# Optimization experiments

Hardware: AMD Instinct MI355X
Metric: run time of the kernel (lower is better)

Reference implementation:

```python
import jax, jax.numpy as jnp
import numpy as np

N_NODES = 65536
N_EDGES = 524288
N_GRAPHS = 512
G_NODES = 10000
NUM_DISEASES = 2000
IN_DIM = 128
HID = 256  # 2 * IN_DIM (z_emb concat feat)
D_FEAT = 512
C_FEAT = 512
MAX_Z = 4000


def setup_inputs() -> dict:
    key = jax.random.key(0)
    ks = jax.random.split(key, 20)
    rn = lambda k, shape: jax.random.normal(k, shape, dtype=jnp.float32) * 0.05
    return {
        "z": jax.random.randint(ks[0], (N_NODES,), 0, MAX_Z),
        "node_id": jnp.sort(jax.random.randint(ks[1], (N_NODES,), 0, G_NODES)),
        "src": jax.random.randint(ks[2], (N_EDGES,), 0, N_NODES),
        "dst": jax.random.randint(ks[3], (N_EDGES,), 0, N_NODES),
        "graph_ids": jnp.sort(jax.random.randint(ks[4], (N_NODES,), 0, N_GRAPHS)),
        "z_table": rn(ks[5], (MAX_Z, IN_DIM)),
        "d_feat_tab": rn(ks[6], (G_NODES, D_FEAT)),
        "c_feat_tab": rn(ks[7], (G_NODES, C_FEAT)),
        "Wd": rn(ks[8], (D_FEAT, IN_DIM)),
        "Wc": rn(ks[9], (C_FEAT, IN_DIM)),
        "gin_W1": rn(ks[10], (HID, HID)), "gin_b1": jnp.zeros((HID,), jnp.float32),
        "gin_W2": rn(ks[11], (HID, HID)), "gin_b2": jnp.zeros((HID,), jnp.float32),
        "sage_Wself": rn(ks[12], (HID, HID)),
        "sage_Wneigh": rn(ks[13], (HID, HID)),
        "sage_b": jnp.zeros((HID,), jnp.float32),
        "lin1_W": rn(ks[14], (HID, HID)), "lin1_b": jnp.zeros((HID,), jnp.float32),
        "lin2_W": rn(ks[15], (HID, 1)), "lin2_b": jnp.zeros((1,), jnp.float32),
    }


def reference(z, node_id, src, dst, graph_ids, z_table, d_feat_tab, c_feat_tab,
              Wd, Wc, gin_W1, gin_b1, gin_W2, gin_b2,
              sage_Wself, sage_Wneigh, sage_b, lin1_W, lin1_b, lin2_W, lin2_b):
    # --- input feature construction (Model.forward) ---
    z_emb = z_table[z]                               # [N, IN_DIM]
    d_proj = d_feat_tab[node_id] @ Wd                # d_fc (bias=False)
    c_proj = c_feat_tab[node_id] @ Wc                # c_fc (bias=False)
    disease = (node_id <= NUM_DISEASES)[:, None]
    # node_id is sorted -> masked concat order == node order
    feat = jnp.where(disease, d_proj, c_proj)        # [N, IN_DIM]
    x = jnp.concatenate([z_emb, feat], axis=1)       # [N, HID]
    # --- GINConv: sum aggregation, eps=0, mlp = Lin->ReLU->Lin ---
    agg = jax.ops.segment_sum(x[src], dst, num_segments=N_NODES)
    h = x + agg
    h = jax.nn.relu(h @ gin_W1 + gin_b1) @ gin_W2 + gin_b2
    # --- SAGEConv('mean'): fc_self(h) + fc_neigh(mean_neighbors) + bias ---
    deg = jax.ops.segment_sum(jnp.ones((N_EDGES,), h.dtype), dst, num_segments=N_NODES)
    mean_n = jax.ops.segment_sum(h[src], dst, num_segments=N_NODES) / jnp.maximum(deg, 1.0)[:, None]
    h = h @ sage_Wself + mean_n @ sage_Wneigh + sage_b
    # --- per-graph max pooling readout ---
    g = jax.ops.segment_max(h, graph_ids, num_segments=N_GRAPHS, indices_are_sorted=True)
    g = jnp.where(jnp.isfinite(g), g, 0.0)           # guard empty graphs
    # --- head: Linear -> ReLU -> (dropout p=0, eval) -> Linear ---
    h = jax.nn.relu(g @ lin1_W + lin1_b)
    return h @ lin2_W + lin2_b                       # [N_GRAPHS, 1]
```

## Files before the change

### kernel.cpp

```cpp
#include <hip/hip_runtime.h>
#include <hip/hip_bf16.h>

#define N_NODES     65536
#define N_EDGES     524288
#define N_GRAPHS    512
#define G_NODES_N   10000
#define NUM_DIS     2000
#define IN_DIM      128
#define HID         256
#define D_FEAT      512

typedef _Float16 half8 __attribute__((ext_vector_type(8)));
typedef _Float16 half4v __attribute__((ext_vector_type(4)));
typedef float    f32x4 __attribute__((ext_vector_type(4)));

__global__ __launch_bounds__(256) void wcvt_all_kernel(
    const float* __restrict__ W1, const float* __restrict__ W2,
    const float* __restrict__ Ws, const float* __restrict__ Wn,
    const float* __restrict__ Wd, const float* __restrict__ Wc,
    _Float16* __restrict__ W1T, _Float16* __restrict__ W2T,
    _Float16* __restrict__ WsT, _Float16* __restrict__ WnT,
    _Float16* __restrict__ WdT, _Float16* __restrict__ WcT)
{
    int b = blockIdx.x;
    const float* W; _Float16* T; int N, K, n;
    if (b < 1024) {
        const int m = b >> 8; n = b & 255; N = HID; K = HID;
        W = (m == 0) ? W1 : (m == 1) ? W2 : (m == 2) ? Ws : Wn;
        T = (m == 0) ? W1T : (m == 1) ? W2T : (m == 2) ? WsT : WnT;
    } else {
        b -= 1024; const int m = b >> 7; n = b & 127; N = IN_DIM; K = D_FEAT;
        W = (m == 0) ? Wd : Wc;
        T = (m == 0) ? WdT : WcT;
    }
    for (int k = threadIdx.x; k < K; k += 256)
        T[(size_t)n * K + k] = (_Float16)W[(size_t)k * N + n];
}

__global__ __launch_bounds__(256) void proj_mfma_kernel(
    const float* __restrict__ dtab, const float* __restrict__ ctab,
    const _Float16* __restrict__ WdT, const _Float16* __restrict__ WcT,
    _Float16* __restrict__ proj)
{
    __shared__ _Float16 Alds[128 * 40];
    __shared__ _Float16 Blds[128 * 40];
    const int blk = blockIdx.x;
    const float* tab; const _Float16* WT; int base, M, bm;
    if (blk < 16) { tab = dtab; WT = WdT; base = 0;           M = NUM_DIS + 1;             bm = blk * 128; }
    else          { tab = ctab; WT = WcT; base = NUM_DIS + 1; M = G_NODES_N - NUM_DIS - 1; bm = (blk - 16) * 128; }
    const int tid  = threadIdx.x;
    const int wave = tid >> 6, lane = tid & 63;
    const int q    = lane >> 4, l16 = lane & 15;
    const int mbase = (wave & 1) * 64, nbase = (wave >> 1) * 64;
    const int r = tid >> 1, s = tid & 1;

    f32x4 acc[4][4] = {};

    for (int kc = 0; kc < 16; ++kc) {
        const int k0 = kc * 32;
        const int arow = min(bm + r, M - 1);
        const float* gA = tab + (size_t)(base + arow) * D_FEAT + k0 + s * 16;
        const _Float16* gB = WT + (size_t)r * D_FEAT + k0 + s * 16;
        const float4 f0 = ((const float4*)gA)[0];
        const float4 f1 = ((const float4*)gA)[1];
        const float4 f2 = ((const float4*)gA)[2];
        const float4 f3 = ((const float4*)gA)[3];
        const half8 hb0 = *(const half8*)gB;
        const half8 hb1 = *(const half8*)(gB + 8);
        half8 h0, h1;
        h0[0]=(_Float16)f0.x; h0[1]=(_Float16)f0.y; h0[2]=(_Float16)f0.z; h0[3]=(_Float16)f0.w;
        h0[4]=(_Float16)f1.x; h0[5]=(_Float16)f1.y; h0[6]=(_Float16)f1.z; h0[7]=(_Float16)f1.w;
        h1[0]=(_Float16)f2.x; h1[1]=(_Float16)f2.y; h1[2]=(_Float16)f2.z; h1[3]=(_Float16)f2.w;
        h1[4]=(_Float16)f3.x; h1[5]=(_Float16)f3.y; h1[6]=(_Float16)f3.z; h1[7]=(_Float16)f3.w;
        __syncthreads();
        *(half8*)&Alds[r * 40 + s * 16]     = h0;
        *(half8*)&Alds[r * 40 + s * 16 + 8] = h1;
        *(half8*)&Blds[r * 40 + s * 16]     = hb0;
        *(half8*)&Blds[r * 40 + s * 16 + 8] = hb1;
        __syncthreads();
        half8 a[4], b[4];
        #pragma unroll
        for (int i = 0; i < 4; ++i)
            a[i] = *(const half8*)&Alds[(mbase + i * 16 + l16) * 40 + q * 8];
        #pragma unroll
        for (int j = 0; j < 4; ++j)
            b[j] = *(const half8*)&Blds[(nbase + j * 16 + l16) * 40 + q * 8];
        #pragma unroll
        for (int i = 0; i < 4; ++i)
            #pragma unroll
            for (int j = 0; j < 4; ++j)
                acc[i][j] = __builtin_amdgcn_mfma_f32_16x16x32_f16(a[i], b[j], acc[i][j], 0, 0, 0);
    }

    #pragma unroll
    for (int j = 0; j < 4; ++j) {
        const int colg = nbase + j * 16 + l16;
        #pragma unroll
        for (int i = 0; i < 4; ++i) {
            #pragma unroll
            for (int rr = 0; rr < 4; ++rr) {
                const int row = bm + mbase + i * 16 + q * 4 + rr;
                if (row < M)
                    proj[(size_t)(base + row) * IN_DIM + colg] = (_Float16)acc[i][j][rr];
            }
        }
    }
}

__global__ __launch_bounds__(256) void build_x_kernel(
    const int* __restrict__ z, const int* __restrict__ node_id,
    const float* __restrict__ z_table, const _Float16* __restrict__ proj,
    _Float16* __restrict__ X)
{
    const int t = blockIdx.x * 256 + threadIdx.x;
    const int node = t >> 6;
    const int q    = t & 63;
    half4v h;
    if (q < 32) {
        const float4 v = ((const float4*)(z_table + (size_t)z[node] * IN_DIM))[q];
        h[0] = (_Float16)v.x; h[1] = (_Float16)v.y;
        h[2] = (_Float16)v.z; h[3] = (_Float16)v.w;
    } else {
        h = *(const half4v*)(proj + (size_t)node_id[node] * IN_DIM + (q - 32) * 4);
    }
    *(half4v*)(X + (size_t)node * HID + q * 4) = h;
}

__global__ __launch_bounds__(256) void hist_kernel(
    const int* __restrict__ dst, int* __restrict__ cnt)
{
    const int e = blockIdx.x * 256 + threadIdx.x;
    if (e < N_EDGES) atomicAdd(&cnt[dst[e]], 1);
}

__global__ __launch_bounds__(256) void seg_sum_kernel(
    const int* __restrict__ cnt, int* __restrict__ seg)
{
    __shared__ int red[256];
    const int t = threadIdx.x;
    const int4 c = *(const int4*)(cnt + blockIdx.x * 1024 + t * 4);
    red[t] = c.x + c.y + c.z + c.w;
    __syncthreads();
    for (int s = 128; s > 0; s >>= 1) {
        if (t < s) red[t] += red[t + s];
        __syncthreads();
    }
    if (t == 0) seg[blockIdx.x] = red[0];
}

__global__ __launch_bounds__(64) void seg_scan_kernel(
    const int* __restrict__ seg, int* __restrict__ segoff,
    int* __restrict__ total_out)
{
    __shared__ int a[64], b[64];
    const int t = threadIdx.x;
    const int v = seg[t];
    a[t] = v;
    __syncthreads();
    int* in = a; int* out = b;
    for (int off = 1; off < 64; off <<= 1) {
        out[t] = in[t] + ((t >= off) ? in[t - off] : 0);
        __syncthreads();
        int* tmp = in; in = out; out = tmp;
    }
    segoff[t] = in[t] - v;
    if (t == 63) total_out[0] = in[63];
}

__global__ __launch_bounds__(256) void local_scan_kernel(
    const int* __restrict__ cnt, const int* __restrict__ segoff,
    int* __restrict__ row_ptr, int* __restrict__ fill)
{
    __shared__ int a[256], b[256];
    const int t = threadIdx.x;
    const int base = blockIdx.x * 1024 + t * 4;
    const int4 c = *(const int4*)(cnt + base);
    const int s = c.x + c.y + c.z + c.w;
    a[t] = s;
    __syncthreads();
    int* in = a; int* out = b;
    for (int off = 1; off < 256; off <<= 1) {
        out[t] = in[t] + ((t >= off) ? in[t - off] : 0);
        __syncthreads();
        int* tmp = in; in = out; out = tmp;
    }
    const int run = in[t] - s + segoff[blockIdx.x];
    int4 r;
    r.x = run; r.y = run + c.x; r.z = r.y + c.y; r.w = r.z + c.z;
    *(int4*)(row_ptr + base) = r;
    *(int4*)(fill + base) = r;
}

__global__ __launch_bounds__(256) void scatter_kernel(
    const int* __restrict__ src, const int* __restrict__ dst,
    int* __restrict__ fill, int* __restrict__ col)
{
    const int e = blockIdx.x * 256 + threadIdx.x;
    if (e < N_EDGES) {
        const int pos = atomicAdd(&fill[dst[e]], 1);
        col[pos] = src[e];
    }
}

__global__ __launch_bounds__(256) void csr_agg_kernel(
    const int* __restrict__ row_ptr, const int* __restrict__ col,
    const _Float16* __restrict__ F, const _Float16* __restrict__ Self,
    _Float16* __restrict__ OUT, const int mean_mode)
{
    const int t = blockIdx.x * 256 + threadIdx.x;
    const int d = t >> 5;
    const int q = t & 31;
    const int beg = row_ptr[d];
    const int end = row_ptr[d + 1];
    float acc[8] = {0.f,0.f,0.f,0.f,0.f,0.f,0.f,0.f};
    if (Self) {
        const half8 sv = *(const half8*)(Self + (size_t)d * HID + q * 8);
        #pragma unroll
        for (int i = 0; i < 8; ++i) acc[i] = (float)sv[i];
    }
    int e = beg;
    for (; e + 4 <= end; e += 4) {
        const int s0 = col[e],     s1 = col[e + 1];
        const int s2 = col[e + 2], s3 = col[e + 3];
        const half8 v0 = *(const half8*)(F + (size_t)s0 * HID + q * 8);
        const half8 v1 = *(const half8*)(F + (size_t)s1 * HID + q * 8);
        const half8 v2 = *(const half8*)(F + (size_t)s2 * HID + q * 8);
        const half8 v3 = *(const half8*)(F + (size_t)s3 * HID + q * 8);
        #pragma unroll
        for (int i = 0; i < 8; ++i)
            acc[i] += ((float)v0[i] + (float)v1[i]) + ((float)v2[i] + (float)v3[i]);
    }
    for (; e < end; ++e) {
        const half8 v0 = *(const half8*)(F + (size_t)col[e] * HID + q * 8);
        #pragma unroll
        for (int i = 0; i < 8; ++i) acc[i] += (float)v0[i];
    }
    if (mean_mode) {
        const float rs = 1.0f / fmaxf((float)(end - beg), 1.0f);
        #pragma unroll
        for (int i = 0; i < 8; ++i) acc[i] *= rs;
    }
    half8 o;
    #pragma unroll
    for (int i = 0; i < 8; ++i) o[i] = (_Float16)acc[i];
    *(half8*)(OUT + (size_t)d * HID + q * 8) = o;
}

__global__ __launch_bounds__(256) void mfma_gemm_kernel(
    const _Float16* __restrict__ A1, const _Float16* __restrict__ A2,
    const _Float16* __restrict__ B1T, const _Float16* __restrict__ B2T,
    const float* __restrict__ bias, _Float16* __restrict__ Ch, const int relu)
{
    __shared__ _Float16 Alds[128 * 40];
    __shared__ _Float16 Blds[128 * 40];
    const int bm   = blockIdx.x * 128;
    const int bn   = blockIdx.y * 128;
    const int tid  = threadIdx.x;
    const int wave = tid >> 6, lane = tid & 63;
    const int q    = lane >> 4, l16 = lane & 15;
    const int mbase = (wave & 1) * 64, nbase = (wave >> 1) * 64;
    const int r = tid >> 1, s = tid & 1;

    f32x4 acc[4][4] = {};
    const int nchunks = A2 ? 16 : 8;

    for (int kc = 0; kc < nchunks; ++kc) {
        const int k0 = (kc & 7) * 32;
        const _Float16* gA = ((kc < 8) ? A1 : A2) + (size_t)(bm + r) * HID + k0 + s * 16;
        const _Float16* gB = ((kc < 8) ? B1T : B2T) + (size_t)(bn + r) * HID + k0 + s * 16;
        const half8 a0 = *(const half8*)gA;
        const half8 a1 = *(const half8*)(gA + 8);
        const half8 b0 = *(const half8*)gB;
        const half8 b1 = *(const half8*)(gB + 8);
        __syncthreads();
        *(half8*)&Alds[r * 40 + s * 16]     = a0;
        *(half8*)&Alds[r * 40 + s * 16 + 8] = a1;
        *(half8*)&Blds[r * 40 + s * 16]     = b0;
        *(half8*)&Blds[r * 40 + s * 16 + 8] = b1;
        __syncthreads();
        half8 a[4], b[4];
        #pragma unroll
        for (int i = 0; i < 4; ++i)
            a[i] = *(const half8*)&Alds[(mbase + i * 16 + l16) * 40 + q * 8];
        #pragma unroll
        for (int j = 0; j < 4; ++j)
            b[j] = *(const half8*)&Blds[(nbase + j * 16 + l16) * 40 + q * 8];
        #pragma unroll
        for (int i = 0; i < 4; ++i)
            #pragma unroll
            for (int j = 0; j < 4; ++j)
                acc[i][j] = __builtin_amdgcn_mfma_f32_16x16x32_f16(a[i], b[j], acc[i][j], 0, 0, 0);
    }

    #pragma unroll
    for (int j = 0; j < 4; ++j) {
        const int colg = bn + nbase + j * 16 + l16;
        const float bv = bias ? bias[colg] : 0.0f;
        #pragma unroll
        for (int i = 0; i < 4; ++i) {
            #pragma unroll
            for (int rr = 0; rr < 4; ++rr) {
                const int rowg = bm + mbase + i * 16 + q * 4 + rr;
                float v = acc[i][j][rr] + bv;
                if (relu) v = fmaxf(v, 0.0f);
                Ch[(size_t)rowg * HID + colg] = (_Float16)v;
            }
        }
    }
}

__global__ __launch_bounds__(256) void pool_head_kernel(
    const _Float16* __restrict__ H2, const int* __restrict__ gid,
    const float* __restrict__ W1, const float* __restrict__ b1,
    const float* __restrict__ W2, const float* __restrict__ b2,
    float* __restrict__ out)
{
    const int g = blockIdx.x;
    const int j = threadIdx.x;
    __shared__ float row[HID];
    __shared__ float red[HID];
    int lo = 0, hi = N_NODES;
    while (lo < hi) { const int mid = (lo + hi) >> 1; if (gid[mid] < g) lo = mid + 1; else hi = mid; }
    const int start = lo;
    hi = N_NODES;
    while (lo < hi) { const int mid = (lo + hi) >> 1; if (gid[mid] < g + 1) lo = mid + 1; else hi = mid; }
    const int end = lo;
    float m = -INFINITY;
    for (int i = start; i < end; ++i)
        m = fmaxf(m, (float)H2[(size_t)i * HID + j]);
    row[j] = (m == -INFINITY) ? 0.0f : m;
    __syncthreads();
    float acc = b1[j];
    for (int k = 0; k < HID; ++k)
        acc = fmaf(row[k], W1[k * HID + j], acc);
    acc = fmaxf(acc, 0.f);
    red[j] = acc * W2[j];
    __syncthreads();
    for (int s = 128; s > 0; s >>= 1) {
        if (j < s) red[j] += red[j + s];
        __syncthreads();
    }
    if (j == 0) out[g] = red[0] + b2[0];
}

extern "C" void kernel_launch(void* const* d_in, const int* in_sizes, int n_in,
                              void* d_out, int out_size, void* d_ws, size_t ws_size,
                              hipStream_t stream)
{
    const int*   z         = (const int*)d_in[0];
    const int*   node_id   = (const int*)d_in[1];
    const int*   src       = (const int*)d_in[2];
    const int*   dst       = (const int*)d_in[3];
    const int*   graph_ids = (const int*)d_in[4];
    const float* z_table   = (const float*)d_in[5];
    const float* d_feat    = (const float*)d_in[6];
    const float* c_feat    = (const float*)d_in[7];
    const float* Wd        = (const float*)d_in[8];
    const float* Wc        = (const float*)d_in[9];
    const float* gin_W1    = (const float*)d_in[10];
    const float* gin_b1    = (const float*)d_in[11];
    const float* gin_W2    = (const float*)d_in[12];
    const float* gin_b2    = (const float*)d_in[13];
    const float* sage_Wself  = (const float*)d_in[14];
    const float* sage_Wneigh = (const float*)d_in[15];
    const float* sage_b    = (const float*)d_in[16];
    const float* lin1_W    = (const float*)d_in[17];
    const float* lin1_b    = (const float*)d_in[18];
    const float* lin2_W    = (const float*)d_in[19];
    const float* lin2_b    = (const float*)d_in[20];
    float* out = (float*)d_out;

    const size_t NH = (size_t)N_NODES * HID;
    char* wsb = (char*)d_ws;
    _Float16* bufA = (_Float16*)wsb;                     wsb += NH * 2;
    _Float16* AGGh = (_Float16*)wsb;                     wsb += NH * 2;
    _Float16* H1h  = (_Float16*)wsb;                     wsb += NH * 2;
    _Float16* projh= (_Float16*)wsb;                     wsb += (size_t)G_NODES_N * IN_DIM * 2;
    _Float16* W1T  = (_Float16*)wsb;                     wsb += HID * HID * 2;
    _Float16* W2T  = (_Float16*)wsb;                     wsb += HID * HID * 2;
    _Float16* WsT  = (_Float16*)wsb;                     wsb += HID * HID * 2;
    _Float16* WnT  = (_Float16*)wsb;                     wsb += HID * HID * 2;
    _Float16* WdT  = (_Float16*)wsb;                     wsb += D_FEAT * IN_DIM * 2;
    _Float16* WcT  = (_Float16*)wsb;                     wsb += D_FEAT * IN_DIM * 2;
    int* row_ptr   = (int*)wsb;                          wsb += (N_NODES + 4) * 4;
    int* cnt       = (int*)wsb;                          wsb += N_NODES * 4;
    int* fill      = (int*)wsb;                          wsb += N_NODES * 4;
    int* col       = (int*)wsb;                          wsb += N_EDGES * 4;
    int* seg       = (int*)wsb;                          wsb += 64 * 4;
    int* segoff    = (int*)wsb;                          wsb += 64 * 4;

    _Float16* Xh  = bufA;
    _Float16* Hh  = bufA;
    _Float16* H2h = H1h;

    hipMemsetAsync(cnt, 0, N_NODES * sizeof(int), stream);
    hist_kernel<<<N_EDGES / 256, 256, 0, stream>>>(dst, cnt);
    seg_sum_kernel<<<64, 256, 0, stream>>>(cnt, seg);
    seg_scan_kernel<<<1, 64, 0, stream>>>(seg, segoff, &row_ptr[N_NODES]);
    local_scan_kernel<<<64, 256, 0, stream>>>(cnt, segoff, row_ptr, fill);
    scatter_kernel<<<N_EDGES / 256, 256, 0, stream>>>(src, dst, fill, col);

    wcvt_all_kernel<<<1280, 256, 0, stream>>>(gin_W1, gin_W2, sage_Wself, sage_Wneigh,
                                              Wd, Wc, W1T, W2T, WsT, WnT, WdT, WcT);

    proj_mfma_kernel<<<16 + 63, 256, 0, stream>>>(d_feat, c_feat, WdT, WcT, projh);

    build_x_kernel<<<(N_NODES * 64) / 256, 256, 0, stream>>>(z, node_id, z_table, projh, Xh);

    csr_agg_kernel<<<(N_NODES * 32) / 256, 256, 0, stream>>>(row_ptr, col, Xh, Xh, AGGh, 0);

    dim3 ggrid(N_NODES / 128, HID / 128);
    mfma_gemm_kernel<<<ggrid, 256, 0, stream>>>(AGGh, nullptr, W1T, nullptr, gin_b1, H1h, 1);
    mfma_gemm_kernel<<<ggrid, 256, 0, stream>>>(H1h, nullptr, W2T, nullptr, gin_b2, Hh, 0);

    csr_agg_kernel<<<(N_NODES * 32) / 256, 256, 0, stream>>>(row_ptr, col, Hh, nullptr, AGGh, 1);

    mfma_gemm_kernel<<<ggrid, 256, 0, stream>>>(Hh, AGGh, WsT, WnT, sage_b, H2h, 0);

    pool_head_kernel<<<N_GRAPHS, 256, 0, stream>>>(H2h, graph_ids, lin1_W, lin1_b,
                                                   lin2_W, lin2_b, out);
}
```

Baseline: 427.0 us.

## Tile weight transpose, use direct global-to-LDS loads in GEMM, split pooling

The weight-conversion kernel now transposes through a 64x64 shared-memory tile, so both reads and writes are coalesced and far fewer blocks are launched. The GEMM stages A and B tiles with global_load_lds straight into an unpadded LDS layout instead of going through registers. Max-pooling is split across 8 blocks per graph, with a separate head kernel that reduces the partial maxima. The unpadded 32-wide LDS rows may raise bank conflicts on the MFMA operand reads, and the extra kernel launch plus partial buffer add some overhead.

```diff
diff --git a/kernel.cpp b/kernel.cpp
--- a/kernel.cpp
+++ b/kernel.cpp
@@ -9,10 +9,14 @@
 #define IN_DIM      128
 #define HID         256
 #define D_FEAT      512
+#define POOL_SPLIT  8
 
 typedef _Float16 half8 __attribute__((ext_vector_type(8)));
 typedef _Float16 half4v __attribute__((ext_vector_type(4)));
 typedef float    f32x4 __attribute__((ext_vector_type(4)));
+
+typedef __attribute__((address_space(1))) const void as1_void;
+typedef __attribute__((address_space(3))) void       as3_void;
 
 __global__ __launch_bounds__(256) void wcvt_all_kernel(
     const float* __restrict__ W1, const float* __restrict__ W2,
@@ -22,19 +26,27 @@
     _Float16* __restrict__ WsT, _Float16* __restrict__ WnT,
     _Float16* __restrict__ WdT, _Float16* __restrict__ WcT)
 {
-    int b = blockIdx.x;
-    const float* W; _Float16* T; int N, K, n;
-    if (b < 1024) {
-        const int m = b >> 8; n = b & 255; N = HID; K = HID;
-        W = (m == 0) ? W1 : (m == 1) ? W2 : (m == 2) ? Ws : Wn;
-        T = (m == 0) ? W1T : (m == 1) ? W2T : (m == 2) ? WsT : WnT;
+    __shared__ float tile[64][65];
+    const int b = blockIdx.x;
+    const int mat = b >> 4, t = b & 15;
+    const float* W; _Float16* T; int K, N, k0, n0;
+    if (mat < 4) {
+        K = HID; N = HID; k0 = (t >> 2) * 64; n0 = (t & 3) * 64;
+        W = (mat == 0) ? W1 : (mat == 1) ? W2 : (mat == 2) ? Ws : Wn;
+        T = (mat == 0) ? W1T : (mat == 1) ? W2T : (mat == 2) ? WsT : WnT;
     } else {
-        b -= 1024; const int m = b >> 7; n = b & 127; N = IN_DIM; K = D_FEAT;
-        W = (m == 0) ? Wd : Wc;
-        T = (m == 0) ? WdT : WcT;
-    }
-    for (int k = threadIdx.x; k < K; k += 256)
-        T[(size_t)n * K + k] = (_Float16)W[(size_t)k * N + n];
+        K = D_FEAT; N = IN_DIM; k0 = (t >> 1) * 64; n0 = (t & 1) * 64;
+        W = (mat == 4) ? Wd : Wc;
+        T = (mat == 4) ? WdT : WcT;
+    }
+    const int tx = threadIdx.x & 63, ty = threadIdx.x >> 6;
+    #pragma unroll
+    for (int r = 0; r < 64; r += 4)
+        tile[r + ty][tx] = W[(size_t)(k0 + r + ty) * N + n0 + tx];
+    __syncthreads();
+    #pragma unroll
+    for (int c = 0; c < 64; c += 4)
+        T[(size_t)(n0 + c + ty) * K + k0 + tx] = (_Float16)tile[tx][c + ty];
 }
 
 __global__ __launch_bounds__(256) void proj_mfma_kernel(
@@ -251,40 +263,42 @@
     const _Float16* __restrict__ B1T, const _Float16* __restrict__ B2T,
     const float* __restrict__ bias, _Float16* __restrict__ Ch, const int relu)
 {
-    __shared__ _Float16 Alds[128 * 40];
-    __shared__ _Float16 Blds[128 * 40];
+    __shared__ _Float16 Alds[128 * 32];
+    __shared__ _Float16 Blds[128 * 32];
     const int bm   = blockIdx.x * 128;
     const int bn   = blockIdx.y * 128;
     const int tid  = threadIdx.x;
     const int wave = tid >> 6, lane = tid & 63;
     const int q    = lane >> 4, l16 = lane & 15;
     const int mbase = (wave & 1) * 64, nbase = (wave >> 1) * 64;
-    const int r = tid >> 1, s = tid & 1;
 
     f32x4 acc[4][4] = {};
     const int nchunks = A2 ? 16 : 8;
 
     for (int kc = 0; kc < nchunks; ++kc) {
         const int k0 = (kc & 7) * 32;
-        const _Float16* gA = ((kc < 8) ? A1 : A2) + (size_t)(bm + r) * HID + k0 + s * 16;
-        const _Float16* gB = ((kc < 8) ? B1T : B2T) + (size_t)(bn + r) * HID + k0 + s * 16;
-        const half8 a0 = *(const half8*)gA;
-        const half8 a1 = *(const half8*)(gA + 8);
-        const half8 b0 = *(const half8*)gB;
-        const half8 b1 = *(const half8*)(gB + 8);
-        __syncthreads();
-        *(half8*)&Alds[r * 40 + s * 16]     = a0;
-        *(half8*)&Alds[r * 40 + s * 16 + 8] = a1;
-        *(half8*)&Blds[r * 40 + s * 16]     = b0;
-        *(half8*)&Blds[r * 40 + s * 16 + 8] = b1;
+        const _Float16* Abase = (kc < 8) ? A1 : A2;
+        const _Float16* Bbase = (kc < 8) ? B1T : B2T;
+        __syncthreads();
+        #pragma unroll
+        for (int t = 0; t < 2; ++t) {
+            const int i   = wave * 128 + t * 64 + lane;
+            const int row = i >> 2, s = i & 3;
+            const _Float16* gA = Abase + (size_t)(bm + row) * HID + k0 + s * 8;
+            const _Float16* gB = Bbase + (size_t)(bn + row) * HID + k0 + s * 8;
+            __builtin_amdgcn_global_load_lds(
+                (as1_void*)gA, (as3_void*)&Alds[(wave * 128 + t * 64) * 8], 16, 0, 0);
+            __builtin_amdgcn_global_load_lds(
+                (as1_void*)gB, (as3_void*)&Blds[(wave * 128 + t * 64) * 8], 16, 0, 0);
+        }
         __syncthreads();
         half8 a[4], b[4];
         #pragma unroll
         for (int i = 0; i < 4; ++i)
-            a[i] = *(const half8*)&Alds[(mbase + i * 16 + l16) * 40 + q * 8];
+            a[i] = *(const half8*)&Alds[(mbase + i * 16 + l16) * 32 + q * 8];
         #pragma unroll
         for (int j = 0; j < 4; ++j)
-            b[j] = *(const half8*)&Blds[(nbase + j * 16 + l16) * 40 + q * 8];
+            b[j] = *(const half8*)&Blds[(nbase + j * 16 + l16) * 32 + q * 8];
         #pragma unroll
         for (int i = 0; i < 4; ++i)
             #pragma unroll
@@ -309,16 +323,13 @@
     }
 }
 
-__global__ __launch_bounds__(256) void pool_head_kernel(
+__global__ __launch_bounds__(256) void pool_part_kernel(
     const _Float16* __restrict__ H2, const int* __restrict__ gid,
-    const float* __restrict__ W1, const float* __restrict__ b1,
-    const float* __restrict__ W2, const float* __restrict__ b2,
-    float* __restrict__ out)
-{
-    const int g = blockIdx.x;
+    float* __restrict__ Gpart)
+{
+    const int g = blockIdx.y;
+    const int sp = blockIdx.x;
     const int j = threadIdx.x;
-    __shared__ float row[HID];
-    __shared__ float red[HID];
     int lo = 0, hi = N_NODES;
     while (lo < hi) { const int mid = (lo + hi) >> 1; if (gid[mid] < g) lo = mid + 1; else hi = mid; }
     const int start = lo;
@@ -326,11 +337,29 @@
     while (lo < hi) { const int mid = (lo + hi) >> 1; if (gid[mid] < g + 1) lo = mid + 1; else hi = mid; }
     const int end = lo;
     float m = -INFINITY;
-    for (int i = start; i < end; ++i)
+    for (int i = start + sp; i < end; i += POOL_SPLIT)
         m = fmaxf(m, (float)H2[(size_t)i * HID + j]);
+    Gpart[((size_t)g * POOL_SPLIT + sp) * HID + j] = m;
+}
+
+__global__ __launch_bounds__(256) void head_kernel(
+    const float* __restrict__ Gpart,
+    const float* __restrict__ W1, const float* __restrict__ b1,
+    const float* __restrict__ W2, const float* __restrict__ b2,
+    float* __restrict__ out)
+{
+    const int g = blockIdx.x;
+    const int j = threadIdx.x;
+    __shared__ float row[HID];
+    __shared__ float red[HID];
+    float m = -INFINITY;
+    #pragma unroll
+    for (int sp = 0; sp < POOL_SPLIT; ++sp)
+        m = fmaxf(m, Gpart[((size_t)g * POOL_SPLIT + sp) * HID + j]);
     row[j] = (m == -INFINITY) ? 0.0f : m;
     __syncthreads();
     float acc = b1[j];
+    #pragma unroll 8
     for (int k = 0; k < HID; ++k)
         acc = fmaf(row[k], W1[k * HID + j], acc);
     acc = fmaxf(acc, 0.f);
@@ -382,6 +411,7 @@
     _Float16* WnT  = (_Float16*)wsb;                     wsb += HID * HID * 2;
     _Float16* WdT  = (_Float16*)wsb;                     wsb += D_FEAT * IN_DIM * 2;
     _Float16* WcT  = (_Float16*)wsb;                     wsb += D_FEAT * IN_DIM * 2;
+    float* Gpart   = (float*)wsb;                        wsb += (size_t)N_GRAPHS * POOL_SPLIT * HID * 4;
     int* row_ptr   = (int*)wsb;                          wsb += (N_NODES + 4) * 4;
     int* cnt       = (int*)wsb;                          wsb += N_NODES * 4;
     int* fill      = (int*)wsb;                          wsb += N_NODES * 4;
@@ -400,8 +430,8 @@
     local_scan_kernel<<<64, 256, 0, stream>>>(cnt, segoff, row_ptr, fill);
     scatter_kernel<<<N_EDGES / 256, 256, 0, stream>>>(src, dst, fill, col);
 
-    wcvt_all_kernel<<<1280, 256, 0, stream>>>(gin_W1, gin_W2, sage_Wself, sage_Wneigh,
-                                              Wd, Wc, W1T, W2T, WsT, WnT, WdT, WcT);
+    wcvt_all_kernel<<<96, 256, 0, stream>>>(gin_W1, gin_W2, sage_Wself, sage_Wneigh,
+                                            Wd, Wc, W1T, W2T, WsT, WnT, WdT, WcT);
 
     proj_mfma_kernel<<<16 + 63, 256, 0, stream>>>(d_feat, c_feat, WdT, WcT, projh);
 
@@ -417,6 +447,7 @@
 
     mfma_gemm_kernel<<<ggrid, 256, 0, stream>>>(Hh, AGGh, WsT, WnT, sage_b, H2h, 0);
 
-    pool_head_kernel<<<N_GRAPHS, 256, 0, stream>>>(H2h, graph_ids, lin1_W, lin1_b,
-                                                   lin2_W, lin2_b, out);
-}
+    dim3 pgrid(POOL_SPLIT, N_GRAPHS);
+    pool_part_kernel<<<pgrid, 256, 0, stream>>>(H2h, graph_ids, Gpart);
+    head_kernel<<<N_GRAPHS, 256, 0, stream>>>(Gpart, lin1_W, lin1_b, lin2_W, lin2_b, out);
+}
```

Result: no change. 428.5 us (+0.4%).
